# Performance work log

Measured on AMD Instinct MI355X. Metric: run time of the kernel, lower is better.

The kernel has to match this reference:

```python
import jax, jax.numpy as jnp
import numpy as np

EMBED_DIM = 1024
NUM_HEADS = 16
HEAD_DIM = EMBED_DIM // NUM_HEADS


def setup_inputs() -> dict:
    key = jax.random.key(0)
    ks = jax.random.split(key, 11)
    B, S, D = 4, 2048, EMBED_DIM
    s = 1.0 / np.sqrt(D)
    return {
        "q": jax.random.normal(ks[0], (B, S, D), jnp.float32),
        "k": jax.random.normal(ks[1], (B, S, D), jnp.float32),
        "v": jax.random.normal(ks[2], (B, S, D), jnp.float32),
        "Wq": jax.random.normal(ks[3], (D, D), jnp.float32) * s,
        "bq": jnp.zeros((D,), jnp.float32),
        "Wk": jax.random.normal(ks[4], (D, D), jnp.float32) * s,
        "bk": jnp.zeros((D,), jnp.float32),
        "Wv": jax.random.normal(ks[5], (D, D), jnp.float32) * s,
        "bv": jnp.zeros((D,), jnp.float32),
        "Wo": jax.random.normal(ks[6], (D, D), jnp.float32) * s,
        "bo": jnp.zeros((D,), jnp.float32),
    }


def reference(q, k, v, Wq, bq, Wk, bk, Wv, bv, Wo, bo):
    B, S, D = q.shape
    H, Hd = NUM_HEADS, HEAD_DIM
    # projections, split heads -> [B, H, S, Hd]
    qh = (q @ Wq + bq).reshape(B, S, H, Hd).transpose(0, 2, 1, 3)
    kh = (k @ Wk + bk).reshape(B, S, H, Hd).transpose(0, 2, 1, 3)
    vh = (v @ Wv + bv).reshape(B, S, H, Hd).transpose(0, 2, 1, 3)
    scale = 1.0 / jnp.sqrt(jnp.asarray(Hd, qh.dtype))
    scores = jnp.einsum('bhqd,bhkd->bhqk', qh, kh) * scale  # [B,H,S,S]
    attn = jax.nn.softmax(scores, axis=-1)  # dropout = identity in eval
    out = jnp.einsum('bhqk,bhkd->bhqd', attn, vh)
    out = out.transpose(0, 2, 1, 3).reshape(B, S, D)
    return out @ Wo + bo
```

## Files before the change

### kernel.cpp

```cpp
#include <hip/hip_runtime.h>

typedef __attribute__((ext_vector_type(8))) __bf16 bf16x8;
typedef __attribute__((ext_vector_type(4))) __bf16 bf16x4;
typedef __attribute__((ext_vector_type(4))) float f32x4;
typedef __attribute__((ext_vector_type(16))) float f32x16;
typedef __attribute__((ext_vector_type(4))) unsigned int u32x4;

#define GLDS(g, l) __builtin_amdgcn_global_load_lds( \
    (const __attribute__((address_space(1))) void*)(g), \
    (__attribute__((address_space(3))) void*)(l), 16, 0, 0)

__device__ __forceinline__ unsigned cvtpk_bf16(float lo, float hi) {
    unsigned r;
    asm("v_cvt_pk_bf16_f32 %0, %1, %2" : "=v"(r) : "v"(lo), "v"(hi));
    return r;
}
__device__ __forceinline__ void pl32swap(unsigned& a, unsigned& b) {
    asm("v_permlane32_swap_b32 %0, %1" : "+v"(a), "+v"(b));
}

__global__ __launch_bounds__(256) void cvt_tile(const float* __restrict__ q,
                                                const float* __restrict__ k,
                                                const float* __restrict__ v,
                                                __bf16* __restrict__ qo,
                                                __bf16* __restrict__ ko,
                                                __bf16* __restrict__ vo) {
    const float* src = blockIdx.z == 0 ? q : blockIdx.z == 1 ? k : v;
    __bf16* dst = blockIdx.z == 0 ? qo : blockIdx.z == 1 ? ko : vo;
    __shared__ __align__(16) __bf16 sb[128 * 64];
    const int t = threadIdx.x;
    const int m0 = blockIdx.x * 128, kk0 = blockIdx.y * 64;
    #pragma unroll
    for (int i = 0; i < 4; i++) {
        int cid = i * 256 + t;
        int r = cid >> 3, cc = cid & 7;
        const float* p = src + (size_t)(m0 + r) * 1024 + kk0 + cc * 8;
        float4 a = *(const float4*)p;
        float4 b2 = *(const float4*)(p + 4);
        bf16x8 o;
        o[0] = (__bf16)a.x;  o[1] = (__bf16)a.y;  o[2] = (__bf16)a.z;  o[3] = (__bf16)a.w;
        o[4] = (__bf16)b2.x; o[5] = (__bf16)b2.y; o[6] = (__bf16)b2.z; o[7] = (__bf16)b2.w;
        *(bf16x8*)((char*)sb + r * 128 + ((cc ^ (r & 7)) << 4)) = o;
    }
    __syncthreads();
    #pragma unroll
    for (int i = 0; i < 4; i++) {
        int cid = i * 256 + t;
        int ch = cid >> 7, r = cid & 127;
        bf16x8 o = *(const bf16x8*)((const char*)sb + r * 128 + ((ch ^ (r & 7)) << 4));
        size_t off = (((size_t)blockIdx.x * 32 + blockIdx.y * 2 + (ch >> 2)) * 4 + (ch & 3)) * 1024
                   + (size_t)r * 8;
        *(bf16x8*)(dst + off) = o;
    }
}

__global__ __launch_bounds__(256) void wtrans2(const float* __restrict__ W,
                                               __bf16* __restrict__ Wt2) {
    __shared__ float lw[64][65];
    const int kt = blockIdx.y * 64, nt = blockIdx.x * 64;
    const int t = threadIdx.x;
    const int r = t >> 4;
    const int c4 = (t & 15) * 4;
    #pragma unroll
    for (int rr = 0; rr < 64; rr += 16) {
        float4 vv = *(const float4*)&W[(size_t)(kt + r + rr) * 1024 + nt + c4];
        lw[r + rr][c4 + 0] = vv.x; lw[r + rr][c4 + 1] = vv.y;
        lw[r + rr][c4 + 2] = vv.z; lw[r + rr][c4 + 3] = vv.w;
    }
    __syncthreads();
    #pragma unroll
    for (int rr = 0; rr < 64; rr += 16) {
        int n = nt + r + rr;
        bf16x4 ov;
        #pragma unroll
        for (int i = 0; i < 4; i++) ov[i] = (__bf16)lw[c4 + i][r + rr];
        int kg = kt + c4;
        size_t off = (((size_t)(n >> 7) * 32 + (kg >> 5)) * 4 + ((kg & 31) >> 3)) * 1024
                   + (size_t)(n & 127) * 8 + (kg & 7);
        *(bf16x4*)&Wt2[off] = ov;
    }
}

template <int OUT>
__global__ __launch_bounds__(256, 2)
void gemm_tt(const __bf16* __restrict__ At, const __bf16* __restrict__ Bt2,
             const float* __restrict__ bias, void* __restrict__ Cout) {
    __shared__ __align__(16) __bf16 sA[3 * 4096];
    __shared__ __align__(16) __bf16 sB[3 * 4096];
    const int t = threadIdx.x, l = t & 63, w = t >> 6;
    const int wr = w >> 1, wc = w & 1;
    const int bid = blockIdx.x, slot = bid >> 3;
    const int ytile = (bid & 7) * 8 + (slot & 7);
    const int xtile = slot >> 3;
    const __bf16* Ab = At + (size_t)ytile * 131072;
    const __bf16* Bb = Bt2 + (size_t)xtile * 131072;

#define GISSUE(ks_, buf_) do { \
    GLDS(Ab + (ks_) * 4096 + t * 8,        (char*)sA + (buf_) * 8192 + t * 16); \
    GLDS(Ab + (ks_) * 4096 + 2048 + t * 8, (char*)sA + (buf_) * 8192 + 4096 + t * 16); \
    GLDS(Bb + (ks_) * 4096 + t * 8,        (char*)sB + (buf_) * 8192 + t * 16); \
    GLDS(Bb + (ks_) * 4096 + 2048 + t * 8, (char*)sB + (buf_) * 8192 + 4096 + t * 16); \
} while (0)

    f32x4 acc[4][4];
    #pragma unroll
    for (int i = 0; i < 4; i++)
        #pragma unroll
        for (int j = 0; j < 4; j++) acc[i][j] = (f32x4){0.f, 0.f, 0.f, 0.f};

    GISSUE(0, 0);
    GISSUE(1, 1);
    int cur = 0;
    #pragma unroll 1
    for (int ks = 0; ks < 32; ++ks) {
        if (ks < 31) asm volatile("s_waitcnt vmcnt(4)" ::: "memory");
        else         asm volatile("s_waitcnt vmcnt(0)" ::: "memory");
        __builtin_amdgcn_s_barrier();
        __builtin_amdgcn_sched_barrier(0);
        const __bf16* bA = sA + cur * 4096;
        const __bf16* bB = sB + cur * 4096;
        bf16x8 af[4], bfr[4];
        #pragma unroll
        for (int i = 0; i < 4; i++)
            af[i] = *(const bf16x8*)(bA + (l >> 4) * 1024 + (wr * 64 + i * 16 + (l & 15)) * 8);
        #pragma unroll
        for (int j = 0; j < 4; j++)
            bfr[j] = *(const bf16x8*)(bB + (l >> 4) * 1024 + (wc * 64 + j * 16 + (l & 15)) * 8);
        #pragma unroll
        for (int i = 0; i < 4; i++)
            #pragma unroll
            for (int j = 0; j < 4; j++)
                acc[i][j] = __builtin_amdgcn_mfma_f32_16x16x32_bf16(af[i], bfr[j], acc[i][j], 0, 0, 0);
        if (ks + 2 < 32) GISSUE(ks + 2, cur >= 1 ? cur - 1 : 2);
        cur = cur == 2 ? 0 : cur + 1;
    }
#undef GISSUE

    const int m0 = ytile * 128, n0 = xtile * 128;
    #pragma unroll
    for (int j = 0; j < 4; j++) {
        int col = n0 + wc * 64 + j * 16 + (l & 15);
        float bv = bias[col];
        #pragma unroll
        for (int i = 0; i < 4; i++) {
            #pragma unroll
            for (int r = 0; r < 4; r++) {
                int row = m0 + wr * 64 + i * 16 + (l >> 4) * 4 + r;
                float vvv = acc[i][j][r] + bv;
                if (OUT == 0) {
                    ((float*)Cout)[(size_t)row * 1024 + col] = vvv;
                } else if (OUT == 1) {
                    ((__bf16*)Cout)[(size_t)row * 1024 + col] = (__bf16)(vvv * 0.18033688f);
                } else if (OUT == 2) {
                    int b_ = row >> 11, s_ = row & 2047, h_ = col >> 6, hd_ = col & 63;
                    size_t off = ((size_t)(b_ * 16 + h_) * 32 + (s_ >> 6)) * 4096
                               + (size_t)(hd_ >> 3) * 512 + (s_ & 63) * 8 + (hd_ & 7);
                    ((__bf16*)Cout)[off] = (__bf16)vvv;
                } else {
                    int b_ = row >> 11, s_ = row & 2047, h_ = col >> 6, d_ = col & 63;
                    size_t off = ((size_t)(b_ * 16 + h_) * 32 + (s_ >> 6)) * 4096
                               + (size_t)((s_ & 63) >> 3) * 512 + (size_t)d_ * 8 + (s_ & 7);
                    ((__bf16*)Cout)[off] = (__bf16)vvv;
                }
            }
        }
    }
}

__global__ __launch_bounds__(256, 2)
void attn_fwd(const __bf16* __restrict__ Qp, const __bf16* __restrict__ Kt,
              const __bf16* __restrict__ Vtt, __bf16* __restrict__ AOt) {
    constexpr int S = 2048, D = 1024;
    __shared__ __align__(16) __bf16 sK[3 * 4096];
    __shared__ __align__(16) __bf16 sV[3 * 4096];
    __shared__ float sL[4][64];
    const int t = threadIdx.x, l = t & 63, w = t >> 6;
    const int c = l & 31, g = l >> 5;
    const int bid = blockIdx.x, slot = bid >> 3;
    const int bh = (slot >> 3) * 8 + (bid & 7);
    const int qb = slot & 7;
    const int b = bh >> 4, h = bh & 15;
    const int q0 = qb * 256;
    const __bf16* Kb = Kt + (size_t)bh * 131072;
    const __bf16* Vb = Vtt + (size_t)bh * 131072;

    bf16x8 qf[2][4];
    #pragma unroll
    for (int qh = 0; qh < 2; qh++) {
        const __bf16* qp = Qp + (size_t)(b * S + q0 + w * 64 + qh * 32 + c) * D + h * 64;
        #pragma unroll
        for (int ks = 0; ks < 4; ks++)
            qf[qh][ks] = *(const bf16x8*)(qp + ks * 16 + g * 8);
    }
    asm volatile("s_waitcnt vmcnt(0)" ::: "memory");

#define AISSUE(ti_, buf_) do { \
    GLDS(Kb + (ti_) * 4096 + t * 8,        (char*)sK + (buf_) * 8192 + t * 16); \
    GLDS(Kb + (ti_) * 4096 + 2048 + t * 8, (char*)sK + (buf_) * 8192 + 4096 + t * 16); \
    GLDS(Vb + (ti_) * 4096 + t * 8,        (char*)sV + (buf_) * 8192 + t * 16); \
    GLDS(Vb + (ti_) * 4096 + 2048 + t * 8, (char*)sV + (buf_) * 8192 + 4096 + t * 16); \
} while (0)

    f32x16 acc[2][2];
    acc[0][0] = (f32x16){}; acc[0][1] = (f32x16){};
    acc[1][0] = (f32x16){}; acc[1][1] = (f32x16){};
    float ls[2] = {0.f, 0.f};

    AISSUE(0, 0);
    AISSUE(1, 1);
    int cur = 0;
    #pragma unroll 1
    for (int tile = 0; tile < 32; ++tile) {
        if (tile < 31) asm volatile("s_waitcnt vmcnt(4)" ::: "memory");
        else           asm volatile("s_waitcnt vmcnt(0)" ::: "memory");
        __builtin_amdgcn_s_barrier();
        __builtin_amdgcn_sched_barrier(0);
        const __bf16* bK = sK + cur * 4096;
        const __bf16* bV = sV + cur * 4096;
        #pragma unroll
        for (int kt = 0; kt < 2; kt++) {
            bf16x8 kf[4];
            #pragma unroll
            for (int ks = 0; ks < 4; ks++)
                kf[ks] = *(const bf16x8*)(bK + ((2 * ks + g) * 64 + kt * 32 + c) * 8);
            bf16x8 vq0[2], vq1[2];
            #pragma unroll
            for (int ti = 0; ti < 2; ti++) {
                vq0[ti] = *(const bf16x8*)(bV + ((4 * kt + g) * 64 + ti * 32 + c) * 8);
                vq1[ti] = *(const bf16x8*)(bV + ((4 * kt + 2 + g) * 64 + ti * 32 + c) * 8);
            }
            #pragma unroll
            for (int qh = 0; qh < 2; qh++) {
                f32x16 St = {};
                St = __builtin_amdgcn_mfma_f32_32x32x16_bf16(kf[0], qf[qh][0], St, 0, 0, 0);
                St = __builtin_amdgcn_mfma_f32_32x32x16_bf16(kf[1], qf[qh][1], St, 0, 0, 0);
                St = __builtin_amdgcn_mfma_f32_32x32x16_bf16(kf[2], qf[qh][2], St, 0, 0, 0);
                St = __builtin_amdgcn_mfma_f32_32x32x16_bf16(kf[3], qf[qh][3], St, 0, 0, 0);
                #pragma unroll
                for (int r2 = 0; r2 < 16; r2++) {
                    float p = __builtin_amdgcn_exp2f(St[r2]);
                    ls[qh] += p;
                    St[r2] = p;
                }
                unsigned w0 = cvtpk_bf16(St[0], St[1]),   w1 = cvtpk_bf16(St[2], St[3]);
                unsigned w2 = cvtpk_bf16(St[4], St[5]),   w3 = cvtpk_bf16(St[6], St[7]);
                unsigned w4 = cvtpk_bf16(St[8], St[9]),   w5 = cvtpk_bf16(St[10], St[11]);
                unsigned w6 = cvtpk_bf16(St[12], St[13]), w7 = cvtpk_bf16(St[14], St[15]);
                pl32swap(w0, w2); pl32swap(w1, w3);
                pl32swap(w4, w6); pl32swap(w5, w7);
                bf16x8 pa0 = __builtin_bit_cast(bf16x8, (u32x4){w0, w1, w2, w3});
                bf16x8 pa1 = __builtin_bit_cast(bf16x8, (u32x4){w4, w5, w6, w7});
                acc[qh][0] = __builtin_amdgcn_mfma_f32_32x32x16_bf16(pa0, vq0[0], acc[qh][0], 0, 0, 0);
                acc[qh][1] = __builtin_amdgcn_mfma_f32_32x32x16_bf16(pa0, vq0[1], acc[qh][1], 0, 0, 0);
                acc[qh][0] = __builtin_amdgcn_mfma_f32_32x32x16_bf16(pa1, vq1[0], acc[qh][0], 0, 0, 0);
                acc[qh][1] = __builtin_amdgcn_mfma_f32_32x32x16_bf16(pa1, vq1[1], acc[qh][1], 0, 0, 0);
            }
        }
        if (tile + 2 < 32) AISSUE(tile + 2, cur >= 1 ? cur - 1 : 2);
        cur = cur == 2 ? 0 : cur + 1;
    }
#undef AISSUE

    float tt0 = ls[0] + __shfl_xor(ls[0], 32);
    float tt1 = ls[1] + __shfl_xor(ls[1], 32);
    if (l < 32) { sL[w][l] = 1.0f / tt0; sL[w][32 + l] = 1.0f / tt1; }
    __syncthreads();

    #pragma unroll
    for (int qh = 0; qh < 2; qh++)
        #pragma unroll
        for (int rq = 0; rq < 4; rq++)
            #pragma unroll
            for (int rr2 = 0; rr2 < 4; rr2++) {
                int reg = rq * 4 + rr2;
                int rloc = rr2 + 8 * rq + 4 * g;
                float rn = sL[w][qh * 32 + rloc];
                int qloc = w * 64 + qh * 32 + rloc;
                int mt = b * 16 + qb * 2 + (qloc >> 7);
                int mr = qloc & 127;
                size_t base = ((size_t)mt * 32 + h * 2) * 4096 + (size_t)(c >> 3) * 1024
                            + (size_t)mr * 8 + (c & 7);
                AOt[base] = (__bf16)(acc[qh][0][reg] * rn);
                AOt[base + 4096] = (__bf16)(acc[qh][1][reg] * rn);
            }
}

extern "C" void kernel_launch(void* const* d_in, const int* in_sizes, int n_in,
                              void* d_out, int out_size, void* d_ws, size_t ws_size,
                              hipStream_t stream) {
    const float* q  = (const float*)d_in[0];
    const float* k  = (const float*)d_in[1];
    const float* v  = (const float*)d_in[2];
    const float* Wq = (const float*)d_in[3];
    const float* bq = (const float*)d_in[4];
    const float* Wk = (const float*)d_in[5];
    const float* bk = (const float*)d_in[6];
    const float* Wv = (const float*)d_in[7];
    const float* bv = (const float*)d_in[8];
    const float* Wo = (const float*)d_in[9];
    const float* bo = (const float*)d_in[10];

    char* ws = (char*)d_ws;
    const size_t MiB = 1024 * 1024;
    __bf16* Atq = (__bf16*)(ws);
    __bf16* Atk = (__bf16*)(ws + 16 * MiB);
    __bf16* Atv = (__bf16*)(ws + 32 * MiB);
    __bf16* W2q = (__bf16*)(ws + 48 * MiB);
    __bf16* W2k = (__bf16*)(ws + 50 * MiB);
    __bf16* W2v = (__bf16*)(ws + 52 * MiB);
    __bf16* W2o = (__bf16*)(ws + 54 * MiB);
    __bf16* Qp  = (__bf16*)(ws + 56 * MiB);
    __bf16* Kt  = (__bf16*)(ws + 72 * MiB);
    __bf16* Vtt = (__bf16*)(ws + 88 * MiB);
    __bf16* AOt = (__bf16*)(ws);

    cvt_tile<<<dim3(64, 16, 3), 256, 0, stream>>>(q, k, v, Atq, Atk, Atv);

    dim3 wg(16, 16);
    wtrans2<<<wg, 256, 0, stream>>>(Wq, W2q);
    wtrans2<<<wg, 256, 0, stream>>>(Wk, W2k);
    wtrans2<<<wg, 256, 0, stream>>>(Wv, W2v);
    wtrans2<<<wg, 256, 0, stream>>>(Wo, W2o);

    gemm_tt<1><<<512, 256, 0, stream>>>(Atq, W2q, bq, Qp);
    gemm_tt<2><<<512, 256, 0, stream>>>(Atk, W2k, bk, Kt);
    gemm_tt<3><<<512, 256, 0, stream>>>(Atv, W2v, bv, Vtt);

    attn_fwd<<<512, 256, 0, stream>>>(Qp, Kt, Vtt, AOt);

    gemm_tt<0><<<512, 256, 0, stream>>>(AOt, W2o, bo, d_out);
}
```

Baseline: 203.3 us.

## Batch QKV GEMMs into one launch with 256x128 tiles; MFMA row sums in attention

Result: slower. 249.2 us (+22.6%).

```diff
diff --git a/kernel.cpp b/kernel.cpp
--- a/kernel.cpp
+++ b/kernel.cpp
@@ -81,25 +81,36 @@
     }
 }
 
-template <int OUT>
-__global__ __launch_bounds__(256, 2)
-void gemm_tt(const __bf16* __restrict__ At, const __bf16* __restrict__ Bt2,
-             const float* __restrict__ bias, void* __restrict__ Cout) {
-    __shared__ __align__(16) __bf16 sA[3 * 4096];
+__global__ __launch_bounds__(512, 2)
+void gemm_tt(const __bf16* __restrict__ A0, const __bf16* __restrict__ A1,
+             const __bf16* __restrict__ A2,
+             const __bf16* __restrict__ B0, const __bf16* __restrict__ B1,
+             const __bf16* __restrict__ B2,
+             const float* __restrict__ bi0, const float* __restrict__ bi1,
+             const float* __restrict__ bi2,
+             void* __restrict__ C0, void* __restrict__ C1, void* __restrict__ C2,
+             int mode0) {
+    __shared__ __align__(16) __bf16 sA[3 * 8192];
     __shared__ __align__(16) __bf16 sB[3 * 4096];
+    const int y = blockIdx.y;
+    const __bf16* At  = y == 0 ? A0 : y == 1 ? A1 : A2;
+    const __bf16* Bt2 = y == 0 ? B0 : y == 1 ? B1 : B2;
+    const float* bias = y == 0 ? bi0 : y == 1 ? bi1 : bi2;
+    void* Cout        = y == 0 ? C0 : y == 1 ? C1 : C2;
+    const int mode    = y == 0 ? mode0 : y + 1;
+
     const int t = threadIdx.x, l = t & 63, w = t >> 6;
     const int wr = w >> 1, wc = w & 1;
-    const int bid = blockIdx.x, slot = bid >> 3;
-    const int ytile = (bid & 7) * 8 + (slot & 7);
-    const int xtile = slot >> 3;
-    const __bf16* Ab = At + (size_t)ytile * 131072;
+    const int bid = blockIdx.x;
+    const int ytile = (bid & 7) * 4 + ((bid >> 3) & 3);
+    const int xtile = bid >> 5;
+    const __bf16* Ab = At + (size_t)ytile * 262144;
     const __bf16* Bb = Bt2 + (size_t)xtile * 131072;
 
 #define GISSUE(ks_, buf_) do { \
-    GLDS(Ab + (ks_) * 4096 + t * 8,        (char*)sA + (buf_) * 8192 + t * 16); \
-    GLDS(Ab + (ks_) * 4096 + 2048 + t * 8, (char*)sA + (buf_) * 8192 + 4096 + t * 16); \
-    GLDS(Bb + (ks_) * 4096 + t * 8,        (char*)sB + (buf_) * 8192 + t * 16); \
-    GLDS(Bb + (ks_) * 4096 + 2048 + t * 8, (char*)sB + (buf_) * 8192 + 4096 + t * 16); \
+    GLDS(Ab + (ks_) * 4096 + t * 8,          (char*)sA + (buf_) * 16384 + t * 16); \
+    GLDS(Ab + 131072 + (ks_) * 4096 + t * 8, (char*)sA + (buf_) * 16384 + 8192 + t * 16); \
+    GLDS(Bb + (ks_) * 4096 + t * 8,          (char*)sB + (buf_) * 8192 + t * 16); \
 } while (0)
 
     f32x4 acc[4][4];
@@ -113,30 +124,33 @@
     int cur = 0;
     #pragma unroll 1
     for (int ks = 0; ks < 32; ++ks) {
-        if (ks < 31) asm volatile("s_waitcnt vmcnt(4)" ::: "memory");
+        if (ks < 31) asm volatile("s_waitcnt vmcnt(3)" ::: "memory");
         else         asm volatile("s_waitcnt vmcnt(0)" ::: "memory");
         __builtin_amdgcn_s_barrier();
         __builtin_amdgcn_sched_barrier(0);
-        const __bf16* bA = sA + cur * 4096;
+        if (ks + 2 < 32) GISSUE(ks + 2, cur >= 1 ? cur - 1 : 2);
+        const __bf16* bA = sA + cur * 8192;
         const __bf16* bB = sB + cur * 4096;
         bf16x8 af[4], bfr[4];
         #pragma unroll
         for (int i = 0; i < 4; i++)
-            af[i] = *(const bf16x8*)(bA + (l >> 4) * 1024 + (wr * 64 + i * 16 + (l & 15)) * 8);
+            af[i] = *(const bf16x8*)(bA + (wr >> 1) * 4096 + (l >> 4) * 1024
+                                        + ((wr & 1) * 64 + i * 16 + (l & 15)) * 8);
         #pragma unroll
         for (int j = 0; j < 4; j++)
             bfr[j] = *(const bf16x8*)(bB + (l >> 4) * 1024 + (wc * 64 + j * 16 + (l & 15)) * 8);
+        __builtin_amdgcn_s_setprio(1);
         #pragma unroll
         for (int i = 0; i < 4; i++)
             #pragma unroll
             for (int j = 0; j < 4; j++)
                 acc[i][j] = __builtin_amdgcn_mfma_f32_16x16x32_bf16(af[i], bfr[j], acc[i][j], 0, 0, 0);
-        if (ks + 2 < 32) GISSUE(ks + 2, cur >= 1 ? cur - 1 : 2);
+        __builtin_amdgcn_s_setprio(0);
         cur = cur == 2 ? 0 : cur + 1;
     }
 #undef GISSUE
 
-    const int m0 = ytile * 128, n0 = xtile * 128;
+    const int m0 = ytile * 256, n0 = xtile * 128;
     #pragma unroll
     for (int j = 0; j < 4; j++) {
         int col = n0 + wc * 64 + j * 16 + (l & 15);
@@ -147,11 +161,11 @@
             for (int r = 0; r < 4; r++) {
                 int row = m0 + wr * 64 + i * 16 + (l >> 4) * 4 + r;
                 float vvv = acc[i][j][r] + bv;
-                if (OUT == 0) {
+                if (mode == 0) {
                     ((float*)Cout)[(size_t)row * 1024 + col] = vvv;
-                } else if (OUT == 1) {
+                } else if (mode == 1) {
                     ((__bf16*)Cout)[(size_t)row * 1024 + col] = (__bf16)(vvv * 0.18033688f);
-                } else if (OUT == 2) {
+                } else if (mode == 2) {
                     int b_ = row >> 11, s_ = row & 2047, h_ = col >> 6, hd_ = col & 63;
                     size_t off = ((size_t)(b_ * 16 + h_) * 32 + (s_ >> 6)) * 4096
                                + (size_t)(hd_ >> 3) * 512 + (s_ & 63) * 8 + (hd_ & 7);
@@ -173,7 +187,6 @@
     constexpr int S = 2048, D = 1024;
     __shared__ __align__(16) __bf16 sK[3 * 4096];
     __shared__ __align__(16) __bf16 sV[3 * 4096];
-    __shared__ float sL[4][64];
     const int t = threadIdx.x, l = t & 63, w = t >> 6;
     const int c = l & 31, g = l >> 5;
     const int bid = blockIdx.x, slot = bid >> 3;
@@ -192,6 +205,8 @@
         for (int ks = 0; ks < 4; ks++)
             qf[qh][ks] = *(const bf16x8*)(qp + ks * 16 + g * 8);
     }
+    const __bf16 one = (__bf16)1.0f;
+    const bf16x8 ones = {one, one, one, one, one, one, one, one};
     asm volatile("s_waitcnt vmcnt(0)" ::: "memory");
 
 #define AISSUE(ti_, buf_) do { \
@@ -204,7 +219,8 @@
     f32x16 acc[2][2];
     acc[0][0] = (f32x16){}; acc[0][1] = (f32x16){};
     acc[1][0] = (f32x16){}; acc[1][1] = (f32x16){};
-    float ls[2] = {0.f, 0.f};
+    f32x16 accl[2];
+    accl[0] = (f32x16){}; accl[1] = (f32x16){};
 
     AISSUE(0, 0);
     AISSUE(1, 1);
@@ -215,6 +231,7 @@
         else           asm volatile("s_waitcnt vmcnt(0)" ::: "memory");
         __builtin_amdgcn_s_barrier();
         __builtin_amdgcn_sched_barrier(0);
+        if (tile + 2 < 32) AISSUE(tile + 2, cur >= 1 ? cur - 1 : 2);
         const __bf16* bK = sK + cur * 4096;
         const __bf16* bV = sV + cur * 4096;
         #pragma unroll
@@ -232,16 +249,15 @@
             #pragma unroll
             for (int qh = 0; qh < 2; qh++) {
                 f32x16 St = {};
+                __builtin_amdgcn_s_setprio(1);
                 St = __builtin_amdgcn_mfma_f32_32x32x16_bf16(kf[0], qf[qh][0], St, 0, 0, 0);
                 St = __builtin_amdgcn_mfma_f32_32x32x16_bf16(kf[1], qf[qh][1], St, 0, 0, 0);
                 St = __builtin_amdgcn_mfma_f32_32x32x16_bf16(kf[2], qf[qh][2], St, 0, 0, 0);
                 St = __builtin_amdgcn_mfma_f32_32x32x16_bf16(kf[3], qf[qh][3], St, 0, 0, 0);
+                __builtin_amdgcn_s_setprio(0);
                 #pragma unroll
-                for (int r2 = 0; r2 < 16; r2++) {
-                    float p = __builtin_amdgcn_exp2f(St[r2]);
-                    ls[qh] += p;
-                    St[r2] = p;
-                }
+                for (int r2 = 0; r2 < 16; r2++)
+                    St[r2] = __builtin_amdgcn_exp2f(St[r2]);
                 unsigned w0 = cvtpk_bf16(St[0], St[1]),   w1 = cvtpk_bf16(St[2], St[3]);
                 unsigned w2 = cvtpk_bf16(St[4], St[5]),   w3 = cvtpk_bf16(St[6], St[7]);
                 unsigned w4 = cvtpk_bf16(St[8], St[9]),   w5 = cvtpk_bf16(St[10], St[11]);
@@ -250,21 +266,19 @@
                 pl32swap(w4, w6); pl32swap(w5, w7);
                 bf16x8 pa0 = __builtin_bit_cast(bf16x8, (u32x4){w0, w1, w2, w3});
                 bf16x8 pa1 = __builtin_bit_cast(bf16x8, (u32x4){w4, w5, w6, w7});
+                __builtin_amdgcn_s_setprio(1);
                 acc[qh][0] = __builtin_amdgcn_mfma_f32_32x32x16_bf16(pa0, vq0[0], acc[qh][0], 0, 0, 0);
                 acc[qh][1] = __builtin_amdgcn_mfma_f32_32x32x16_bf16(pa0, vq0[1], acc[qh][1], 0, 0, 0);
                 acc[qh][0] = __builtin_amdgcn_mfma_f32_32x32x16_bf16(pa1, vq1[0], acc[qh][0], 0, 0, 0);
                 acc[qh][1] = __builtin_amdgcn_mfma_f32_32x32x16_bf16(pa1, vq1[1], acc[qh][1], 0, 0, 0);
+                accl[qh] = __builtin_amdgcn_mfma_f32_32x32x16_bf16(pa0, ones, accl[qh], 0, 0, 0);
+                accl[qh] = __builtin_amdgcn_mfma_f32_32x32x16_bf16(pa1, ones, accl[qh], 0, 0, 0);
+                __builtin_amdgcn_s_setprio(0);
             }
         }
-        if (tile + 2 < 32) AISSUE(tile + 2, cur >= 1 ? cur - 1 : 2);
         cur = cur == 2 ? 0 : cur + 1;
     }
 #undef AISSUE
-
-    float tt0 = ls[0] + __shfl_xor(ls[0], 32);
-    float tt1 = ls[1] + __shfl_xor(ls[1], 32);
-    if (l < 32) { sL[w][l] = 1.0f / tt0; sL[w][32 + l] = 1.0f / tt1; }
-    __syncthreads();
 
     #pragma unroll
     for (int qh = 0; qh < 2; qh++)
@@ -274,7 +288,7 @@
             for (int rr2 = 0; rr2 < 4; rr2++) {
                 int reg = rq * 4 + rr2;
                 int rloc = rr2 + 8 * rq + 4 * g;
-                float rn = sL[w][qh * 32 + rloc];
+                float rn = __builtin_amdgcn_rcpf(accl[qh][reg]);
                 int qloc = w * 64 + qh * 32 + rloc;
                 int mt = b * 16 + qb * 2 + (qloc >> 7);
                 int mr = qloc & 127;
@@ -322,11 +336,11 @@
     wtrans2<<<wg, 256, 0, stream>>>(Wv, W2v);
     wtrans2<<<wg, 256, 0, stream>>>(Wo, W2o);
 
-    gemm_tt<1><<<512, 256, 0, stream>>>(Atq, W2q, bq, Qp);
-    gemm_tt<2><<<512, 256, 0, stream>>>(Atk, W2k, bk, Kt);
-    gemm_tt<3><<<512, 256, 0, stream>>>(Atv, W2v, bv, Vtt);
+    gemm_tt<<<dim3(256, 3), 512, 0, stream>>>(Atq, Atk, Atv, W2q, W2k, W2v,
+                                              bq, bk, bv, Qp, Kt, Vtt, 1);
 
     attn_fwd<<<512, 256, 0, stream>>>(Qp, Kt, Vtt, AOt);
 
-    gemm_tt<0><<<512, 256, 0, stream>>>(AOt, W2o, bo, d_out);
-}
+    gemm_tt<<<dim3(256, 1), 512, 0, stream>>>(AOt, AOt, AOt, W2o, W2o, W2o,
+                                              bo, bo, bo, d_out, d_out, d_out, 0);
+}
```
